# Performance work log

Hardware: AMD Instinct MI355X
Metric: run time of the kernel (lower is better)

Reference implementation:

```python
import jax, jax.numpy as jnp
import numpy as np

DIM = 1024
NUM_HEADS = 16
HEAD_DIM = DIM // NUM_HEADS

def setup_inputs() -> dict:
    key = jax.random.key(0)
    ks = jax.random.split(key, 5)
    s = 1.0 / np.sqrt(DIM)
    x = jax.random.normal(ks[0], (2, 2048, DIM), dtype=jnp.float32)
    W_qkv = jax.random.uniform(ks[1], (DIM, 3 * DIM), dtype=jnp.float32, minval=-s, maxval=s)
    b_qkv = jax.random.uniform(ks[2], (3 * DIM,), dtype=jnp.float32, minval=-s, maxval=s)
    W_out = jax.random.uniform(ks[3], (DIM, DIM), dtype=jnp.float32, minval=-s, maxval=s)
    b_out = jax.random.uniform(ks[4], (DIM,), dtype=jnp.float32, minval=-s, maxval=s)
    return {"x": x, "W_qkv": W_qkv, "b_qkv": b_qkv, "W_out": W_out, "b_out": b_out}

def reference(x, W_qkv, b_qkv, W_out, b_out):
    B, S, _ = x.shape
    qkv = x @ W_qkv + b_qkv                       # [B,S,3*dim]
    q, k, v = jnp.split(qkv, 3, axis=-1)
    # [B,S,dim] -> [B,H,S,hd]
    def to_heads(t):
        return t.reshape(B, S, NUM_HEADS, HEAD_DIM).transpose(0, 2, 1, 3)
    q, k, v = to_heads(q), to_heads(k), to_heads(v)
    scale = HEAD_DIM ** -0.5
    scores = jnp.einsum('bhqd,bhkd->bhqk', q, k) * scale
    attn = jax.nn.softmax(scores, axis=-1)
    out = jnp.einsum('bhqk,bhkd->bhqd', attn, v)  # [B,H,S,hd]
    out = out.transpose(0, 2, 1, 3).reshape(B, S, DIM)
    return out @ W_out + b_out
```

## Files before the change

### kernel.cpp

```cpp
#include <hip/hip_runtime.h>
#include <math.h>

#define DIMM    1024
#define NHEADS  16
#define HDIM    64
#define BATCH   2
#define SEQ     2048
#define ROWS    (BATCH*SEQ)

typedef _Float16 f16x8 __attribute__((ext_vector_type(8)));
typedef _Float16 f16x4 __attribute__((ext_vector_type(4)));
typedef float    f32x4 __attribute__((ext_vector_type(4)));

__device__ inline void gl_lds16(const void* g, void* l) {
    __builtin_amdgcn_global_load_lds(
        (const __attribute__((address_space(1))) void*)g,
        (__attribute__((address_space(3))) void*)l, 16, 0, 0);
}

__device__ void tcvt64(const float* __restrict__ in, _Float16* __restrict__ out,
                       int K, int N, int k0, int n0, float (*tile)[65], int t)
{
    {
        const int c4 = (t & 15) * 4;
        const int r  = t >> 4;
        #pragma unroll
        for (int i = 0; i < 4; i++) {
            const int rr = r + 16 * i;
            float4 v = *(const float4*)(in + (size_t)(k0 + rr) * N + n0 + c4);
            tile[rr][c4] = v.x; tile[rr][c4 + 1] = v.y;
            tile[rr][c4 + 2] = v.z; tile[rr][c4 + 3] = v.w;
        }
    }
    __syncthreads();
    #pragma unroll
    for (int i = 0; i < 2; i++) {
        const int seg = t + 256 * i;
        const int n   = seg >> 3;
        const int kc  = (seg & 7) * 8;
        f16x8 o;
        #pragma unroll
        for (int j = 0; j < 8; j++) o[j] = (_Float16)tile[kc + j][n];
        *(f16x8*)(out + (size_t)(n0 + n) * K + k0 + kc) = o;
    }
}

__global__ __launch_bounds__(256)
void prep_kernel(const float* __restrict__ x, const float* __restrict__ Wqkv,
                 const float* __restrict__ Wout, _Float16* __restrict__ xh,
                 _Float16* __restrict__ wqkvt, _Float16* __restrict__ woutt)
{
    __shared__ float tile[64][65];
    const int bx = blockIdx.x;
    const int t  = threadIdx.x;
    if (bx < 2048) {
        const int i = bx * 256 + t;
        const float4 a = *(const float4*)(x + (size_t)i * 8);
        const float4 b = *(const float4*)(x + (size_t)i * 8 + 4);
        f16x8 o;
        o[0] = (_Float16)a.x; o[1] = (_Float16)a.y; o[2] = (_Float16)a.z; o[3] = (_Float16)a.w;
        o[4] = (_Float16)b.x; o[5] = (_Float16)b.y; o[6] = (_Float16)b.z; o[7] = (_Float16)b.w;
        *(f16x8*)(xh + (size_t)i * 8) = o;
    } else if (bx < 2816) {
        const int id = bx - 2048;
        const int gx = id % 48, gy = id / 48;
        tcvt64(Wqkv, wqkvt, DIMM, 3 * DIMM, gy * 64, gx * 64, tile, t);
    } else {
        const int id = bx - 2816;
        const int gx = id & 15, gy = id >> 4;
        tcvt64(Wout, woutt, DIMM, DIMM, gy * 64, gx * 64, tile, t);
    }
}

__global__ __launch_bounds__(256)
void vtranspose_kernel(const _Float16* __restrict__ qkvh, _Float16* __restrict__ vt)
{
    __shared__ _Float16 tile[64][72];
    const int kt = blockIdx.x;
    const int bh = blockIdx.y;
    const int b  = bh >> 4, h = bh & 15;
    const int t  = threadIdx.x;
    {
        const int key = t >> 2, c4 = (t & 3) * 16;
        const _Float16* src = qkvh + ((size_t)(b * SEQ + kt * 64 + key)) * (3 * DIMM)
                              + 2 * DIMM + h * HDIM + c4;
        f16x8 v0 = *(const f16x8*)src;
        f16x8 v1 = *(const f16x8*)(src + 8);
        #pragma unroll
        for (int j = 0; j < 8; j++) {
            tile[c4 + j][key]     = v0[j];
            tile[c4 + 8 + j][key] = v1[j];
        }
    }
    __syncthreads();
    {
        const int d = t >> 2, k4 = (t & 3) * 16;
        f16x8 o0, o1;
        #pragma unroll
        for (int j = 0; j < 8; j++) { o0[j] = tile[d][k4 + j]; o1[j] = tile[d][k4 + 8 + j]; }
        _Float16* dst = vt + ((size_t)bh * 64 + d) * SEQ + kt * 64 + k4;
        *(f16x8*)dst       = o0;
        *(f16x8*)(dst + 8) = o1;
    }
}

template<int OUT_F16>
__global__ __launch_bounds__(256)
void hgemm_bias_kernel(const _Float16* __restrict__ A, const _Float16* __restrict__ Bt,
                       const float* __restrict__ bias, void* __restrict__ Cout,
                       int N, int K)
{
    __shared__ _Float16 As[128 * 64];
    __shared__ _Float16 Bs[128 * 64];

    const int t    = threadIdx.x;
    const int w    = t >> 6, lane = t & 63;
    const int quad = lane >> 4, l16 = lane & 15;
    const int wr   = w >> 1, wc = w & 1;
    const int row0 = blockIdx.y * 128, col0 = blockIdx.x * 128;
    const int sw   = l16 & 7;

    f32x4 acc[4][4];
    #pragma unroll
    for (int i = 0; i < 4; i++)
        #pragma unroll
        for (int j = 0; j < 4; j++)
            #pragma unroll
            for (int r = 0; r < 4; r++) acc[i][j][r] = 0.f;

    const _Float16* gA[4];
    const _Float16* gB[4];
    int lofs[4];
    #pragma unroll
    for (int j = 0; j < 4; j++) {
        const int s   = t + 256 * j;
        const int row = s >> 3;
        const int kb  = (s & 7) ^ (row & 7);
        gA[j] = A  + (size_t)(row0 + row) * K + kb * 8;
        gB[j] = Bt + (size_t)(col0 + row) * K + kb * 8;
        lofs[j] = s * 8;
    }

    const int niter = K >> 6;
    #pragma unroll 1
    for (int it = 0; it < niter; it++) {
        __syncthreads();
        #pragma unroll
        for (int j = 0; j < 4; j++) gl_lds16(gA[j], As + lofs[j]);
        #pragma unroll
        for (int j = 0; j < 4; j++) gl_lds16(gB[j], Bs + lofs[j]);
        #pragma unroll
        for (int j = 0; j < 4; j++) { gA[j] += 64; gB[j] += 64; }
        __syncthreads();

        f16x8 af[4][2], bf[4][2];
        #pragma unroll
        for (int i = 0; i < 4; i++) {
            const int arow = wr * 64 + i * 16 + l16;
            const int brow = wc * 64 + i * 16 + l16;
            #pragma unroll
            for (int hh = 0; hh < 2; hh++) {
                af[i][hh] = *(const f16x8*)(As + (arow * 8 + ((hh * 4 + quad) ^ sw)) * 8);
                bf[i][hh] = *(const f16x8*)(Bs + (brow * 8 + ((hh * 4 + quad) ^ sw)) * 8);
            }
        }
        #pragma unroll
        for (int i = 0; i < 4; i++)
            #pragma unroll
            for (int j = 0; j < 4; j++) {
                acc[i][j] = __builtin_amdgcn_mfma_f32_16x16x32_f16(af[i][0], bf[j][0], acc[i][j], 0, 0, 0);
                acc[i][j] = __builtin_amdgcn_mfma_f32_16x16x32_f16(af[i][1], bf[j][1], acc[i][j], 0, 0, 0);
            }
    }

    #pragma unroll
    for (int j = 0; j < 4; j++) {
        const int col = col0 + wc * 64 + j * 16 + l16;
        const float bv = bias[col];
        #pragma unroll
        for (int i = 0; i < 4; i++) {
            const int row = row0 + wr * 64 + i * 16 + quad * 4;
            #pragma unroll
            for (int r = 0; r < 4; r++) {
                const float v = acc[i][j][r] + bv;
                if (OUT_F16)
                    ((_Float16*)Cout)[(size_t)(row + r) * N + col] = (_Float16)v;
                else
                    ((float*)Cout)[(size_t)(row + r) * N + col] = v;
            }
        }
    }
}

__global__ __launch_bounds__(256, 4)
void flash_attn_kernel(const _Float16* __restrict__ qkv,
                       const _Float16* __restrict__ vtg,
                       _Float16* __restrict__ out)
{
    const int qt = blockIdx.x;
    const int bh = blockIdx.y;
    const int b  = bh >> 4, h = bh & 15;
    const int t    = threadIdx.x;
    const int w    = t >> 6;
    const int lane = t & 63;
    const int quad = lane >> 4;
    const int l16  = lane & 15;
    const int sw   = l16 & 7;

    __shared__ __align__(16) _Float16 Ks [2][64 * 64];
    __shared__ __align__(16) _Float16 Vts[2][64 * 64];
    __shared__ __align__(16) _Float16 Ps [64 * 64];

    const int q0 = qt * 64;
    const size_t rstr = 3 * DIMM;
    const _Float16* qbase = qkv + (size_t)b * SEQ * rstr;

    f16x8 qf[4][2];
    #pragma unroll
    for (int qb = 0; qb < 4; qb++) {
        const _Float16* qrow = qbase + (size_t)(q0 + qb * 16 + l16) * rstr + h * HDIM;
        qf[qb][0] = *(const f16x8*)(qrow + quad * 8);
        qf[qb][1] = *(const f16x8*)(qrow + 32 + quad * 8);
    }

    f32x4 Oacc[4];
    #pragma unroll
    for (int i = 0; i < 4; i++) Oacc[i] = (f32x4){0.f, 0.f, 0.f, 0.f};
    float lrow[4] = {0.f, 0.f, 0.f, 0.f};

    const int seg0 = t, seg1 = t + 256;
    const int r0 = seg0 >> 3, lb0 = (seg0 & 7) ^ (r0 & 7);
    const int r1 = seg1 >> 3, lb1 = (seg1 & 7) ^ (r1 & 7);
    const _Float16* gK0 = qbase + (size_t)r0 * rstr + DIMM + h * HDIM + lb0 * 8;
    const _Float16* gK1 = qbase + (size_t)r1 * rstr + DIMM + h * HDIM + lb1 * 8;
    const _Float16* gV0 = vtg + ((size_t)bh * 64 + r0) * SEQ + lb0 * 8;
    const _Float16* gV1 = vtg + ((size_t)bh * 64 + r1) * SEQ + lb1 * 8;

    const int kAbase = (16 * w + l16) * 64;
    const int pRbase = (16 * w + l16) * 64;
    const int pWg = (2 * w + (quad >> 1));
    const int pWo = (quad & 1) * 4;

    gl_lds16(gK0, &Ks [0][seg0 * 8]);
    gl_lds16(gK1, &Ks [0][seg1 * 8]);
    gl_lds16(gV0, &Vts[0][seg0 * 8]);
    gl_lds16(gV1, &Vts[0][seg1 * 8]);

    #pragma unroll 2
    for (int k0 = 0; k0 < SEQ; k0 += 64) {
        const int cur = (k0 >> 6) & 1;
        const _Float16* KsC  = &Ks [cur][0];
        const _Float16* VtsC = &Vts[cur][0];

        if (k0 + 64 < SEQ) {
            const int nxt = cur ^ 1;
            gl_lds16(gK0 + (size_t)(k0 + 64) * rstr, &Ks [nxt][seg0 * 8]);
            gl_lds16(gK1 + (size_t)(k0 + 64) * rstr, &Ks [nxt][seg1 * 8]);
            gl_lds16(gV0 + (k0 + 64),                &Vts[nxt][seg0 * 8]);
            gl_lds16(gV1 + (k0 + 64),                &Vts[nxt][seg1 * 8]);
            asm volatile("s_waitcnt vmcnt(4)" ::: "memory");
        } else {
            asm volatile("s_waitcnt vmcnt(0)" ::: "memory");
        }
        __builtin_amdgcn_s_barrier();
        asm volatile("" ::: "memory");

        f16x8 kf0 = *(const f16x8*)(KsC + kAbase + ((0 + quad) ^ sw) * 8);
        f16x8 kf1 = *(const f16x8*)(KsC + kAbase + ((4 + quad) ^ sw) * 8);
        #pragma unroll
        for (int qb = 0; qb < 4; qb++) {
            f32x4 s = (f32x4){0.f, 0.f, 0.f, 0.f};
            s = __builtin_amdgcn_mfma_f32_16x16x32_f16(kf0, qf[qb][0], s, 0, 0, 0);
            s = __builtin_amdgcn_mfma_f32_16x16x32_f16(kf1, qf[qb][1], s, 0, 0, 0);
            float p0 = __expf(s[0] * 0.125f);
            float p1 = __expf(s[1] * 0.125f);
            float p2 = __expf(s[2] * 0.125f);
            float p3 = __expf(s[3] * 0.125f);
            lrow[qb] += (p0 + p1) + (p2 + p3);
            f16x4 pk;
            pk[0] = (_Float16)p0; pk[1] = (_Float16)p1;
            pk[2] = (_Float16)p2; pk[3] = (_Float16)p3;
            *(f16x4*)(Ps + (qb * 16 + l16) * 64 + (pWg ^ sw) * 8 + pWo) = pk;
        }
        asm volatile("s_waitcnt lgkmcnt(0)" ::: "memory");
        __builtin_amdgcn_s_barrier();
        asm volatile("" ::: "memory");

        f16x8 pf0 = *(const f16x8*)(Ps + pRbase + ((0 + quad) ^ sw) * 8);
        f16x8 pf1 = *(const f16x8*)(Ps + pRbase + ((4 + quad) ^ sw) * 8);
        #pragma unroll
        for (int db = 0; db < 4; db++) {
            const int vrow = db * 16 + l16;
            f16x8 vf0 = *(const f16x8*)(VtsC + vrow * 64 + ((0 + quad) ^ sw) * 8);
            f16x8 vf1 = *(const f16x8*)(VtsC + vrow * 64 + ((4 + quad) ^ sw) * 8);
            Oacc[db] = __builtin_amdgcn_mfma_f32_16x16x32_f16(pf0, vf0, Oacc[db], 0, 0, 0);
            Oacc[db] = __builtin_amdgcn_mfma_f32_16x16x32_f16(pf1, vf1, Oacc[db], 0, 0, 0);
        }
        __builtin_amdgcn_s_barrier();
        asm volatile("" ::: "memory");
    }

    #pragma unroll
    for (int qb = 0; qb < 4; qb++) {
        lrow[qb] += __shfl_xor(lrow[qb], 16);
        lrow[qb] += __shfl_xor(lrow[qb], 32);
    }
    __syncthreads();
    float* lbuf = (float*)Ks;
    if (lane < 16) {
        #pragma unroll
        for (int qb = 0; qb < 4; qb++) lbuf[w * 64 + qb * 16 + lane] = lrow[qb];
    }
    __syncthreads();
    const int qloc = 16 * w + quad * 4;
    float lrec[4];
    #pragma unroll
    for (int r = 0; r < 4; r++) {
        const int q = qloc + r;
        lrec[r] = 1.f / (lbuf[q] + lbuf[64 + q] + lbuf[128 + q] + lbuf[192 + q]);
    }
    #pragma unroll
    for (int db = 0; db < 4; db++) {
        #pragma unroll
        for (int r = 0; r < 4; r++) {
            out[(size_t)(b * SEQ + q0 + qloc + r) * DIMM + h * HDIM + db * 16 + l16] =
                (_Float16)(Oacc[db][r] * lrec[r]);
        }
    }
}

extern "C" void kernel_launch(void* const* d_in, const int* in_sizes, int n_in,
                              void* d_out, int out_size, void* d_ws, size_t ws_size,
                              hipStream_t stream)
{
    const float* x    = (const float*)d_in[0];
    const float* Wqkv = (const float*)d_in[1];
    const float* bqkv = (const float*)d_in[2];
    const float* Wout = (const float*)d_in[3];
    const float* bout = (const float*)d_in[4];
    float* out = (float*)d_out;

    _Float16* qkvh  = (_Float16*)d_ws;
    _Float16* attnh = qkvh  + (size_t)ROWS * 3 * DIMM;
    _Float16* xh    = attnh + (size_t)ROWS * DIMM;
    _Float16* wqkvt = xh    + (size_t)ROWS * DIMM;
    _Float16* woutt = wqkvt + (size_t)3 * DIMM * DIMM;
    _Float16* vtg   = woutt + (size_t)DIMM * DIMM;

    prep_kernel<<<3072, 256, 0, stream>>>(x, Wqkv, Wout, xh, wqkvt, woutt);
    {
        dim3 grid(3 * DIMM / 128, ROWS / 128);
        hgemm_bias_kernel<1><<<grid, 256, 0, stream>>>(xh, wqkvt, bqkv, qkvh, 3 * DIMM, DIMM);
    }
    {
        dim3 grid(SEQ / 64, BATCH * NHEADS);
        vtranspose_kernel<<<grid, 256, 0, stream>>>(qkvh, vtg);
    }
    {
        dim3 grid(SEQ / 64, BATCH * NHEADS);
        flash_attn_kernel<<<grid, 256, 0, stream>>>(qkvh, vtg, attnh);
    }
    {
        dim3 grid(DIMM / 128, ROWS / 128);
        hgemm_bias_kernel<0><<<grid, 256, 0, stream>>>(attnh, woutt, bout, out, DIMM, DIMM);
    }
}
```

Measured before the change: 212.2 us.

## Rework flash attention with 32x32 MFMA, register P shuffle, and split-K waves

Rewrites the attention kernel to use 32x32x16 MFMA tiles, with each wave owning 32 queries and one half of the key block. The P matrix is handed from the score MFMA output to the PV MFMA input through cross-lane shuffles instead of the LDS staging buffer, which removes one barrier per iteration. The two key-half partial O accumulators are combined through LDS at the end. The per-block global prefetch wait structure changes, adding a __syncthreads at loop top and relying on it for load completion, which may affect overlap and correctness of the double buffering.

```diff
diff --git a/kernel.cpp b/kernel.cpp
--- a/kernel.cpp
+++ b/kernel.cpp
@@ -11,11 +11,23 @@
 typedef _Float16 f16x8 __attribute__((ext_vector_type(8)));
 typedef _Float16 f16x4 __attribute__((ext_vector_type(4)));
 typedef float    f32x4 __attribute__((ext_vector_type(4)));
+typedef float    f32x16 __attribute__((ext_vector_type(16)));
 
 __device__ inline void gl_lds16(const void* g, void* l) {
     __builtin_amdgcn_global_load_lds(
         (const __attribute__((address_space(1))) void*)g,
         (__attribute__((address_space(3))) void*)l, 16, 0, 0);
+}
+
+static __device__ inline unsigned packh(_Float16 a, _Float16 b) {
+    unsigned short ua = __builtin_bit_cast(unsigned short, a);
+    unsigned short ub = __builtin_bit_cast(unsigned short, b);
+    return (unsigned)ua | ((unsigned)ub << 16);
+}
+static __device__ inline f16x8 mkfrag(unsigned a, unsigned b, unsigned c, unsigned d) {
+    union { unsigned u[4]; f16x8 v; } x;
+    x.u[0] = a; x.u[1] = b; x.u[2] = c; x.u[3] = d;
+    return x.v;
 }
 
 __device__ void tcvt64(const float* __restrict__ in, _Float16* __restrict__ out,
@@ -199,47 +211,45 @@
 {
     const int qt = blockIdx.x;
     const int bh = blockIdx.y;
-    const int b  = bh >> 4, h = bh & 15;
+    const int b  = bh >> 4, hd = bh & 15;
     const int t    = threadIdx.x;
     const int w    = t >> 6;
     const int lane = t & 63;
-    const int quad = lane >> 4;
-    const int l16  = lane & 15;
-    const int sw   = l16 & 7;
+    const int qg   = w >> 1;
+    const int kh   = w & 1;
+    const int l31  = lane & 31;
+    const int hf   = lane >> 5;
+    const int l7   = lane & 7;
 
     __shared__ __align__(16) _Float16 Ks [2][64 * 64];
     __shared__ __align__(16) _Float16 Vts[2][64 * 64];
-    __shared__ __align__(16) _Float16 Ps [64 * 64];
 
     const int q0 = qt * 64;
     const size_t rstr = 3 * DIMM;
     const _Float16* qbase = qkv + (size_t)b * SEQ * rstr;
 
-    f16x8 qf[4][2];
-    #pragma unroll
-    for (int qb = 0; qb < 4; qb++) {
-        const _Float16* qrow = qbase + (size_t)(q0 + qb * 16 + l16) * rstr + h * HDIM;
-        qf[qb][0] = *(const f16x8*)(qrow + quad * 8);
-        qf[qb][1] = *(const f16x8*)(qrow + 32 + quad * 8);
-    }
-
-    f32x4 Oacc[4];
-    #pragma unroll
-    for (int i = 0; i < 4; i++) Oacc[i] = (f32x4){0.f, 0.f, 0.f, 0.f};
-    float lrow[4] = {0.f, 0.f, 0.f, 0.f};
+    f16x8 qf[4];
+    {
+        const _Float16* qrow = qbase + (size_t)(q0 + qg * 32 + l31) * rstr + hd * HDIM;
+        #pragma unroll
+        for (int dd = 0; dd < 4; dd++)
+            qf[dd] = *(const f16x8*)(qrow + dd * 16 + hf * 8);
+    }
+
+    f32x16 Oacc[2];
+    #pragma unroll
+    for (int dh = 0; dh < 2; dh++)
+        #pragma unroll
+        for (int r = 0; r < 16; r++) Oacc[dh][r] = 0.f;
+    float lrow = 0.f;
 
     const int seg0 = t, seg1 = t + 256;
     const int r0 = seg0 >> 3, lb0 = (seg0 & 7) ^ (r0 & 7);
     const int r1 = seg1 >> 3, lb1 = (seg1 & 7) ^ (r1 & 7);
-    const _Float16* gK0 = qbase + (size_t)r0 * rstr + DIMM + h * HDIM + lb0 * 8;
-    const _Float16* gK1 = qbase + (size_t)r1 * rstr + DIMM + h * HDIM + lb1 * 8;
+    const _Float16* gK0 = qbase + (size_t)r0 * rstr + DIMM + hd * HDIM + lb0 * 8;
+    const _Float16* gK1 = qbase + (size_t)r1 * rstr + DIMM + hd * HDIM + lb1 * 8;
     const _Float16* gV0 = vtg + ((size_t)bh * 64 + r0) * SEQ + lb0 * 8;
     const _Float16* gV1 = vtg + ((size_t)bh * 64 + r1) * SEQ + lb1 * 8;
-
-    const int kAbase = (16 * w + l16) * 64;
-    const int pRbase = (16 * w + l16) * 64;
-    const int pWg = (2 * w + (quad >> 1));
-    const int pWo = (quad & 1) * 4;
 
     gl_lds16(gK0, &Ks [0][seg0 * 8]);
     gl_lds16(gK1, &Ks [0][seg1 * 8]);
@@ -251,6 +261,17 @@
         const int cur = (k0 >> 6) & 1;
         const _Float16* KsC  = &Ks [cur][0];
         const _Float16* VtsC = &Vts[cur][0];
+
+        __syncthreads();
+
+        f32x16 sacc;
+        #pragma unroll
+        for (int r = 0; r < 16; r++) sacc[r] = 0.f;
+        #pragma unroll
+        for (int dd = 0; dd < 4; dd++) {
+            f16x8 kf = *(const f16x8*)(KsC + (kh * 32 + l31) * 64 + (((dd * 2 + hf) ^ l7) * 8));
+            sacc = __builtin_amdgcn_mfma_f32_32x32x16_f16(kf, qf[dd], sacc, 0, 0, 0);
+        }
 
         if (k0 + 64 < SEQ) {
             const int nxt = cur ^ 1;
@@ -258,74 +279,70 @@
             gl_lds16(gK1 + (size_t)(k0 + 64) * rstr, &Ks [nxt][seg1 * 8]);
             gl_lds16(gV0 + (k0 + 64),                &Vts[nxt][seg0 * 8]);
             gl_lds16(gV1 + (k0 + 64),                &Vts[nxt][seg1 * 8]);
-            asm volatile("s_waitcnt vmcnt(4)" ::: "memory");
-        } else {
-            asm volatile("s_waitcnt vmcnt(0)" ::: "memory");
-        }
-        __builtin_amdgcn_s_barrier();
-        asm volatile("" ::: "memory");
-
-        f16x8 kf0 = *(const f16x8*)(KsC + kAbase + ((0 + quad) ^ sw) * 8);
-        f16x8 kf1 = *(const f16x8*)(KsC + kAbase + ((4 + quad) ^ sw) * 8);
-        #pragma unroll
-        for (int qb = 0; qb < 4; qb++) {
-            f32x4 s = (f32x4){0.f, 0.f, 0.f, 0.f};
-            s = __builtin_amdgcn_mfma_f32_16x16x32_f16(kf0, qf[qb][0], s, 0, 0, 0);
-            s = __builtin_amdgcn_mfma_f32_16x16x32_f16(kf1, qf[qb][1], s, 0, 0, 0);
-            float p0 = __expf(s[0] * 0.125f);
-            float p1 = __expf(s[1] * 0.125f);
-            float p2 = __expf(s[2] * 0.125f);
-            float p3 = __expf(s[3] * 0.125f);
-            lrow[qb] += (p0 + p1) + (p2 + p3);
-            f16x4 pk;
-            pk[0] = (_Float16)p0; pk[1] = (_Float16)p1;
-            pk[2] = (_Float16)p2; pk[3] = (_Float16)p3;
-            *(f16x4*)(Ps + (qb * 16 + l16) * 64 + (pWg ^ sw) * 8 + pWo) = pk;
-        }
-        asm volatile("s_waitcnt lgkmcnt(0)" ::: "memory");
-        __builtin_amdgcn_s_barrier();
-        asm volatile("" ::: "memory");
-
-        f16x8 pf0 = *(const f16x8*)(Ps + pRbase + ((0 + quad) ^ sw) * 8);
-        f16x8 pf1 = *(const f16x8*)(Ps + pRbase + ((4 + quad) ^ sw) * 8);
-        #pragma unroll
-        for (int db = 0; db < 4; db++) {
-            const int vrow = db * 16 + l16;
-            f16x8 vf0 = *(const f16x8*)(VtsC + vrow * 64 + ((0 + quad) ^ sw) * 8);
-            f16x8 vf1 = *(const f16x8*)(VtsC + vrow * 64 + ((4 + quad) ^ sw) * 8);
-            Oacc[db] = __builtin_amdgcn_mfma_f32_16x16x32_f16(pf0, vf0, Oacc[db], 0, 0, 0);
-            Oacc[db] = __builtin_amdgcn_mfma_f32_16x16x32_f16(pf1, vf1, Oacc[db], 0, 0, 0);
-        }
-        __builtin_amdgcn_s_barrier();
-        asm volatile("" ::: "memory");
-    }
-
-    #pragma unroll
-    for (int qb = 0; qb < 4; qb++) {
-        lrow[qb] += __shfl_xor(lrow[qb], 16);
-        lrow[qb] += __shfl_xor(lrow[qb], 32);
-    }
+        }
+
+        _Float16 hh[16];
+        #pragma unroll
+        for (int r = 0; r < 16; r++) {
+            const float e = __expf(sacc[r] * 0.125f);
+            hh[r] = (_Float16)e;
+            lrow += (float)hh[r];
+        }
+
+        unsigned w01 = packh(hh[0],  hh[1]),  w23 = packh(hh[2],  hh[3]);
+        unsigned w45 = packh(hh[4],  hh[5]),  w67 = packh(hh[6],  hh[7]);
+        unsigned w89 = packh(hh[8],  hh[9]),  wab = packh(hh[10], hh[11]);
+        unsigned wcd = packh(hh[12], hh[13]), wef = packh(hh[14], hh[15]);
+        unsigned o01 = __shfl_xor((int)w01, 32), o23 = __shfl_xor((int)w23, 32);
+        unsigned o45 = __shfl_xor((int)w45, 32), o67 = __shfl_xor((int)w67, 32);
+        unsigned o89 = __shfl_xor((int)w89, 32), oab = __shfl_xor((int)wab, 32);
+        unsigned ocd = __shfl_xor((int)wcd, 32), oef = __shfl_xor((int)wef, 32);
+        f16x8 pa0 = mkfrag(hf ? o45 : w01, hf ? o67 : w23,
+                           hf ? w45 : o01, hf ? w67 : o23);
+        f16x8 pa1 = mkfrag(hf ? ocd : w89, hf ? oef : wab,
+                           hf ? wcd : o89, hf ? wef : oab);
+
+        #pragma unroll
+        for (int dh = 0; dh < 2; dh++) {
+            const _Float16* vrow = VtsC + (dh * 32 + l31) * 64;
+            f16x8 vf0 = *(const f16x8*)(vrow + (((kh * 4 + 0 + hf) ^ l7) * 8));
+            f16x8 vf1 = *(const f16x8*)(vrow + (((kh * 4 + 2 + hf) ^ l7) * 8));
+            Oacc[dh] = __builtin_amdgcn_mfma_f32_32x32x16_f16(pa0, vf0, Oacc[dh], 0, 0, 0);
+            Oacc[dh] = __builtin_amdgcn_mfma_f32_32x32x16_f16(pa1, vf1, Oacc[dh], 0, 0, 0);
+        }
+    }
+
+    float lsum = lrow + __shfl_xor(lrow, 32);
     __syncthreads();
-    float* lbuf = (float*)Ks;
-    if (lane < 16) {
-        #pragma unroll
-        for (int qb = 0; qb < 4; qb++) lbuf[w * 64 + qb * 16 + lane] = lrow[qb];
+    float* Obuf = (float*)&Ks[0][0];
+    float* lbuf = (float*)&Vts[0][0];
+    if (kh) {
+        #pragma unroll
+        for (int dh = 0; dh < 2; dh++)
+            #pragma unroll
+            for (int r = 0; r < 16; r++) {
+                const int q = (r & 3) + 8 * (r >> 2) + 4 * hf;
+                Obuf[(qg * 32 + q) * 64 + dh * 32 + l31] = Oacc[dh][r];
+            }
+        if (lane < 32) lbuf[qg * 32 + lane] = lsum;
     }
     __syncthreads();
-    const int qloc = 16 * w + quad * 4;
-    float lrec[4];
-    #pragma unroll
-    for (int r = 0; r < 4; r++) {
-        const int q = qloc + r;
-        lrec[r] = 1.f / (lbuf[q] + lbuf[64 + q] + lbuf[128 + q] + lbuf[192 + q]);
-    }
-    #pragma unroll
-    for (int db = 0; db < 4; db++) {
-        #pragma unroll
-        for (int r = 0; r < 4; r++) {
-            out[(size_t)(b * SEQ + q0 + qloc + r) * DIMM + h * HDIM + db * 16 + l16] =
-                (_Float16)(Oacc[db][r] * lrec[r]);
-        }
+    if (!kh) {
+        const float dnrec = 1.f / (lsum + lbuf[qg * 32 + l31]);
+        float dq[16];
+        #pragma unroll
+        for (int r = 0; r < 16; r++)
+            dq[r] = __shfl(dnrec, (r & 3) + 8 * (r >> 2) + 4 * hf);
+        #pragma unroll
+        for (int dh = 0; dh < 2; dh++)
+            #pragma unroll
+            for (int r = 0; r < 16; r++) {
+                const int q = (r & 3) + 8 * (r >> 2) + 4 * hf;
+                const float v = (Oacc[dh][r] + Obuf[(qg * 32 + q) * 64 + dh * 32 + l31])
+                                * dq[r];
+                out[(size_t)(b * SEQ + q0 + qg * 32 + q) * DIMM + hd * HDIM + dh * 32 + l31] =
+                    (_Float16)v;
+            }
     }
 }
 
```

Result: faster. 204.7 us (-3.5%).
